# Kernel optimization log

Measured on AMD Instinct MI355X. Metric: run time of the kernel, lower is better.

The kernel has to match this reference:

```python
import jax, jax.numpy as jnp
import numpy as np

WIN = (9, 9)
EPS = 1e-05
DN = ('NCHW', 'OIHW', 'NCHW')


def _box_sum(x, win):
    # Separable box-sum (mathematically identical to conv2d with an all-ones
    kh = jnp.ones((1, 1, win[0], 1), x.dtype)
    kw = jnp.ones((1, 1, 1, win[1]), x.dtype)
    ph, pw = win[0] // 2, win[1] // 2
    x = jax.lax.conv_general_dilated(x, kh, (1, 1), [(ph, ph), (0, 0)], dimension_numbers=DN)
    x = jax.lax.conv_general_dilated(x, kw, (1, 1), [(0, 0), (pw, pw)], dimension_numbers=DN)
    return x


def setup_inputs() -> dict:
    key = jax.random.key(0)
    k1, k2 = jax.random.split(key)
    I = jax.random.normal(k1, (16, 1, 1024, 1024), dtype=jnp.float32)
    J = jax.random.normal(k2, (16, 1, 1024, 1024), dtype=jnp.float32)
    return {"I": I, "J": J}


def reference(I, J):
    win_size = WIN[0] * WIN[1]  # 81
    I_sum = _box_sum(I, WIN)
    J_sum = _box_sum(J, WIN)
    I2_sum = _box_sum(I * I, WIN)
    J2_sum = _box_sum(J * J, WIN)
    IJ_sum = _box_sum(I * J, WIN)

    u_I = I_sum / win_size
    u_J = J_sum / win_size

    cross = IJ_sum - u_J * I_sum - u_I * J_sum + u_I * u_J * win_size
    I_var = I2_sum - 2.0 * u_I * I_sum + u_I * u_I * win_size
    J_var = J2_sum - 2.0 * u_J * J_sum + u_J * u_J * win_size

    cc = cross * cross / (I_var * J_var + EPS)
    return -1.0 * jnp.mean(cc) + 1.0
```

## Files before the change

### kernel.cpp

```cpp
#include <hip/hip_runtime.h>

#define W_     1024
#define H_     1024
#define NIMG   16
#define HS     32
#define NTHR   128
#define PAD    4
#define CS_N   (W_ + 2*PAD)
#define EPS_   1e-5f
#define VS_LD  1160

__device__ __forceinline__ int swz(int cs) { return cs + (cs >> 3); }

__global__ __launch_bounds__(NTHR) void ncc_main(const float* __restrict__ Iall,
                                                 const float* __restrict__ Jall,
                                                 float* __restrict__ acc)
{
    const int bx    = blockIdx.x;
    const int img   = bx >> 5;
    const int strip = bx & 31;
    const int r0    = strip * HS;
    const int t     = threadIdx.x;

    const float* __restrict__ Ib = Iall + (size_t)img * (W_ * H_);
    const float* __restrict__ Jb = Jall + (size_t)img * (W_ * H_);

    __shared__ float vs[5][VS_LD];

    if (t < 2 * PAD) {
        int cs = (t < PAD) ? t : (CS_N - 2 * PAD + t);
        #pragma unroll
        for (int ch = 0; ch < 5; ++ch) vs[ch][swz(cs)] = 0.0f;
    }

    float sI[8], sJ[8], sII[8], sJJ[8], sIJ[8];
    #pragma unroll
    for (int k = 0; k < 8; ++k) { sI[k]=0.f; sJ[k]=0.f; sII[k]=0.f; sJJ[k]=0.f; sIJ[k]=0.f; }

    for (int q = r0 - PAD; q < r0 + PAD; ++q) {
        if (q >= 0) {
            #pragma unroll
            for (int k = 0; k < 8; ++k) {
                const int c = t + k * NTHR;
                const float a = Ib[q * W_ + c];
                const float b = Jb[q * W_ + c];
                sI[k]+=a; sJ[k]+=b; sII[k]+=a*a; sJJ[k]+=b*b; sIJ[k]+=a*b;
            }
        }
    }
    __syncthreads();

    float accum = 0.0f;
    const float inv81 = 1.0f / 81.0f;

    for (int r = r0; r < r0 + HS; ++r) {
        const int qe = r + PAD;
        if (qe < H_) {
            #pragma unroll
            for (int k = 0; k < 8; ++k) {
                const int c = t + k * NTHR;
                const float a = Ib[qe * W_ + c];
                const float b = Jb[qe * W_ + c];
                sI[k]+=a; sJ[k]+=b; sII[k]+=a*a; sJJ[k]+=b*b; sIJ[k]+=a*b;
            }
        }
        #pragma unroll
        for (int k = 0; k < 8; ++k) {
            const int idx = swz(t + k * NTHR + PAD);
            vs[0][idx] = sI[k];
            vs[1][idx] = sJ[k];
            vs[2][idx] = sII[k];
            vs[3][idx] = sJJ[k];
            vs[4][idx] = sIJ[k];
        }
        __syncthreads();

        float h[5][8];
        {
            const int base = t * 8;
            #pragma unroll
            for (int ch = 0; ch < 5; ++ch) {
                float w[16];
                #pragma unroll
                for (int x = 0; x < 16; ++x) w[x] = vs[ch][swz(base + x)];
                float s = 0.f;
                #pragma unroll
                for (int x = 0; x < 9; ++x) s += w[x];
                h[ch][0] = s;
                #pragma unroll
                for (int c = 1; c < 8; ++c) { s += w[c + 8] - w[c - 1]; h[ch][c] = s; }
            }
        }
        #pragma unroll
        for (int c = 0; c < 8; ++c) {
            const float SI = h[0][c], SJ = h[1][c];
            const float SII = h[2][c], SJJ = h[3][c], SIJ = h[4][c];
            const float cross = SIJ - SI * SJ * inv81;
            const float iv    = SII - SI * SI * inv81;
            const float jv    = SJJ - SJ * SJ * inv81;
            accum += cross * cross / (iv * jv + EPS_);
        }
        __syncthreads();

        const int ql = r - PAD;
        if (ql >= 0 && r + 1 < r0 + HS) {
            #pragma unroll
            for (int k = 0; k < 8; ++k) {
                const int c = t + k * NTHR;
                const float a = Ib[ql * W_ + c];
                const float b = Jb[ql * W_ + c];
                sI[k]-=a; sJ[k]-=b; sII[k]-=a*a; sJJ[k]-=b*b; sIJ[k]-=a*b;
            }
        }
    }

    #pragma unroll
    for (int off = 32; off > 0; off >>= 1) accum += __shfl_down(accum, off);
    if ((t & 63) == 0) atomicAdd(acc, accum);
}

__global__ void ncc_finalize(const float* __restrict__ acc, float* __restrict__ out)
{
    out[0] = 1.0f - acc[0] * (1.0f / (float)((size_t)NIMG * W_ * H_));
}

extern "C" void kernel_launch(void* const* d_in, const int* in_sizes, int n_in,
                              void* d_out, int out_size, void* d_ws, size_t ws_size,
                              hipStream_t stream)
{
    const float* I = (const float*)d_in[0];
    const float* J = (const float*)d_in[1];
    float* acc = (float*)d_ws;

    hipMemsetAsync(acc, 0, sizeof(float), stream);
    ncc_main<<<NIMG * (H_ / HS), NTHR, 0, stream>>>(I, J, acc);
    ncc_finalize<<<1, 1, 0, stream>>>(acc, (float*)d_out);
}
```

Measured before the change: 191.0 us.

## Vectorize global/LDS accesses with contiguous columns, halve strip height, use fast reciprocal

```diff
diff --git a/kernel.cpp b/kernel.cpp
--- a/kernel.cpp
+++ b/kernel.cpp
@@ -3,24 +3,23 @@
 #define W_     1024
 #define H_     1024
 #define NIMG   16
-#define HS     32
+#define HS     16
 #define NTHR   128
 #define PAD    4
-#define CS_N   (W_ + 2*PAD)
 #define EPS_   1e-5f
+__device__ __forceinline__ int f_(int cs) { return cs + ((cs >> 5) << 2); }
 #define VS_LD  1160
 
-__device__ __forceinline__ int swz(int cs) { return cs + (cs >> 3); }
-
-__global__ __launch_bounds__(NTHR) void ncc_main(const float* __restrict__ Iall,
-                                                 const float* __restrict__ Jall,
-                                                 float* __restrict__ acc)
+__global__ __launch_bounds__(NTHR, 2) void ncc_main(const float* __restrict__ Iall,
+                                                    const float* __restrict__ Jall,
+                                                    float* __restrict__ acc)
 {
     const int bx    = blockIdx.x;
-    const int img   = bx >> 5;
-    const int strip = bx & 31;
+    const int img   = bx >> 6;
+    const int strip = bx & 63;
     const int r0    = strip * HS;
     const int t     = threadIdx.x;
+    const int c0    = t * 8;
 
     const float* __restrict__ Ib = Iall + (size_t)img * (W_ * H_);
     const float* __restrict__ Jb = Jall + (size_t)img * (W_ * H_);
@@ -28,9 +27,9 @@
     __shared__ float vs[5][VS_LD];
 
     if (t < 2 * PAD) {
-        int cs = (t < PAD) ? t : (CS_N - 2 * PAD + t);
+        const int cs = (t < PAD) ? t : (1024 + t);
         #pragma unroll
-        for (int ch = 0; ch < 5; ++ch) vs[ch][swz(cs)] = 0.0f;
+        for (int ch = 0; ch < 5; ++ch) vs[ch][f_(cs)] = 0.0f;
     }
 
     float sI[8], sJ[8], sII[8], sJJ[8], sIJ[8];
@@ -39,12 +38,18 @@
 
     for (int q = r0 - PAD; q < r0 + PAD; ++q) {
         if (q >= 0) {
+            const float4 a0 = *reinterpret_cast<const float4*>(Ib + (size_t)q * W_ + c0);
+            const float4 a1 = *reinterpret_cast<const float4*>(Ib + (size_t)q * W_ + c0 + 4);
+            const float4 b0 = *reinterpret_cast<const float4*>(Jb + (size_t)q * W_ + c0);
+            const float4 b1 = *reinterpret_cast<const float4*>(Jb + (size_t)q * W_ + c0 + 4);
+            const float av[8] = {a0.x,a0.y,a0.z,a0.w,a1.x,a1.y,a1.z,a1.w};
+            const float bv[8] = {b0.x,b0.y,b0.z,b0.w,b1.x,b1.y,b1.z,b1.w};
             #pragma unroll
             for (int k = 0; k < 8; ++k) {
-                const int c = t + k * NTHR;
-                const float a = Ib[q * W_ + c];
-                const float b = Jb[q * W_ + c];
-                sI[k]+=a; sJ[k]+=b; sII[k]+=a*a; sJJ[k]+=b*b; sIJ[k]+=a*b;
+                sI[k]+=av[k]; sJ[k]+=bv[k];
+                sII[k]=__builtin_fmaf(av[k],av[k],sII[k]);
+                sJJ[k]=__builtin_fmaf(bv[k],bv[k],sJJ[k]);
+                sIJ[k]=__builtin_fmaf(av[k],bv[k],sIJ[k]);
             }
         }
     }
@@ -53,63 +58,90 @@
     float accum = 0.0f;
     const float inv81 = 1.0f / 81.0f;
 
+    const int wi0 = f_(PAD + c0), wi1 = f_(PAD + c0 + 4);
+    const int ri0 = f_(c0), ri1 = f_(c0 + 4), ri2 = f_(c0 + 8), ri3 = f_(c0 + 12);
+
     for (int r = r0; r < r0 + HS; ++r) {
         const int qe = r + PAD;
         if (qe < H_) {
+            const float4 a0 = *reinterpret_cast<const float4*>(Ib + (size_t)qe * W_ + c0);
+            const float4 a1 = *reinterpret_cast<const float4*>(Ib + (size_t)qe * W_ + c0 + 4);
+            const float4 b0 = *reinterpret_cast<const float4*>(Jb + (size_t)qe * W_ + c0);
+            const float4 b1 = *reinterpret_cast<const float4*>(Jb + (size_t)qe * W_ + c0 + 4);
+            const float av[8] = {a0.x,a0.y,a0.z,a0.w,a1.x,a1.y,a1.z,a1.w};
+            const float bv[8] = {b0.x,b0.y,b0.z,b0.w,b1.x,b1.y,b1.z,b1.w};
             #pragma unroll
             for (int k = 0; k < 8; ++k) {
-                const int c = t + k * NTHR;
-                const float a = Ib[qe * W_ + c];
-                const float b = Jb[qe * W_ + c];
-                sI[k]+=a; sJ[k]+=b; sII[k]+=a*a; sJJ[k]+=b*b; sIJ[k]+=a*b;
+                sI[k]+=av[k]; sJ[k]+=bv[k];
+                sII[k]=__builtin_fmaf(av[k],av[k],sII[k]);
+                sJJ[k]=__builtin_fmaf(bv[k],bv[k],sJJ[k]);
+                sIJ[k]=__builtin_fmaf(av[k],bv[k],sIJ[k]);
             }
         }
-        #pragma unroll
-        for (int k = 0; k < 8; ++k) {
-            const int idx = swz(t + k * NTHR + PAD);
-            vs[0][idx] = sI[k];
-            vs[1][idx] = sJ[k];
-            vs[2][idx] = sII[k];
-            vs[3][idx] = sJJ[k];
-            vs[4][idx] = sIJ[k];
+        {
+            float* p;
+            p = &vs[0][0];
+            *reinterpret_cast<float4*>(p+wi0) = make_float4(sI[0],sI[1],sI[2],sI[3]);
+            *reinterpret_cast<float4*>(p+wi1) = make_float4(sI[4],sI[5],sI[6],sI[7]);
+            p = &vs[1][0];
+            *reinterpret_cast<float4*>(p+wi0) = make_float4(sJ[0],sJ[1],sJ[2],sJ[3]);
+            *reinterpret_cast<float4*>(p+wi1) = make_float4(sJ[4],sJ[5],sJ[6],sJ[7]);
+            p = &vs[2][0];
+            *reinterpret_cast<float4*>(p+wi0) = make_float4(sII[0],sII[1],sII[2],sII[3]);
+            *reinterpret_cast<float4*>(p+wi1) = make_float4(sII[4],sII[5],sII[6],sII[7]);
+            p = &vs[3][0];
+            *reinterpret_cast<float4*>(p+wi0) = make_float4(sJJ[0],sJJ[1],sJJ[2],sJJ[3]);
+            *reinterpret_cast<float4*>(p+wi1) = make_float4(sJJ[4],sJJ[5],sJJ[6],sJJ[7]);
+            p = &vs[4][0];
+            *reinterpret_cast<float4*>(p+wi0) = make_float4(sIJ[0],sIJ[1],sIJ[2],sIJ[3]);
+            *reinterpret_cast<float4*>(p+wi1) = make_float4(sIJ[4],sIJ[5],sIJ[6],sIJ[7]);
         }
         __syncthreads();
 
         float h[5][8];
-        {
-            const int base = t * 8;
+        #pragma unroll
+        for (int ch = 0; ch < 5; ++ch) {
+            const float* p = &vs[ch][0];
+            const float4 w0 = *reinterpret_cast<const float4*>(p + ri0);
+            const float4 w1 = *reinterpret_cast<const float4*>(p + ri1);
+            const float4 w2 = *reinterpret_cast<const float4*>(p + ri2);
+            const float4 w3 = *reinterpret_cast<const float4*>(p + ri3);
+            const float w[16] = {w0.x,w0.y,w0.z,w0.w, w1.x,w1.y,w1.z,w1.w,
+                                 w2.x,w2.y,w2.z,w2.w, w3.x,w3.y,w3.z,w3.w};
+            float s = 0.f;
             #pragma unroll
-            for (int ch = 0; ch < 5; ++ch) {
-                float w[16];
-                #pragma unroll
-                for (int x = 0; x < 16; ++x) w[x] = vs[ch][swz(base + x)];
-                float s = 0.f;
-                #pragma unroll
-                for (int x = 0; x < 9; ++x) s += w[x];
-                h[ch][0] = s;
-                #pragma unroll
-                for (int c = 1; c < 8; ++c) { s += w[c + 8] - w[c - 1]; h[ch][c] = s; }
-            }
+            for (int x = 0; x < 9; ++x) s += w[x];
+            h[ch][0] = s;
+            #pragma unroll
+            for (int c = 1; c < 8; ++c) { s += w[c + 8] - w[c - 1]; h[ch][c] = s; }
         }
         #pragma unroll
         for (int c = 0; c < 8; ++c) {
             const float SI = h[0][c], SJ = h[1][c];
             const float SII = h[2][c], SJJ = h[3][c], SIJ = h[4][c];
-            const float cross = SIJ - SI * SJ * inv81;
-            const float iv    = SII - SI * SI * inv81;
-            const float jv    = SJJ - SJ * SJ * inv81;
-            accum += cross * cross / (iv * jv + EPS_);
+            const float cross = __builtin_fmaf(-SI * SJ, inv81, SIJ);
+            const float iv    = __builtin_fmaf(-SI * SI, inv81, SII);
+            const float jv    = __builtin_fmaf(-SJ * SJ, inv81, SJJ);
+            accum = __builtin_fmaf(cross * cross,
+                                   __builtin_amdgcn_rcpf(__builtin_fmaf(iv, jv, EPS_)),
+                                   accum);
         }
         __syncthreads();
 
         const int ql = r - PAD;
         if (ql >= 0 && r + 1 < r0 + HS) {
+            const float4 a0 = *reinterpret_cast<const float4*>(Ib + (size_t)ql * W_ + c0);
+            const float4 a1 = *reinterpret_cast<const float4*>(Ib + (size_t)ql * W_ + c0 + 4);
+            const float4 b0 = *reinterpret_cast<const float4*>(Jb + (size_t)ql * W_ + c0);
+            const float4 b1 = *reinterpret_cast<const float4*>(Jb + (size_t)ql * W_ + c0 + 4);
+            const float av[8] = {a0.x,a0.y,a0.z,a0.w,a1.x,a1.y,a1.z,a1.w};
+            const float bv[8] = {b0.x,b0.y,b0.z,b0.w,b1.x,b1.y,b1.z,b1.w};
             #pragma unroll
             for (int k = 0; k < 8; ++k) {
-                const int c = t + k * NTHR;
-                const float a = Ib[ql * W_ + c];
-                const float b = Jb[ql * W_ + c];
-                sI[k]-=a; sJ[k]-=b; sII[k]-=a*a; sJJ[k]-=b*b; sIJ[k]-=a*b;
+                sI[k]-=av[k]; sJ[k]-=bv[k];
+                sII[k]=__builtin_fmaf(-av[k],av[k],sII[k]);
+                sJJ[k]=__builtin_fmaf(-bv[k],bv[k],sJJ[k]);
+                sIJ[k]=__builtin_fmaf(-av[k],bv[k],sIJ[k]);
             }
         }
     }
```

New measurement: 185.5 us. 1.03x faster.
